# Performance work log

Hardware: AMD Instinct MI355X
Metric: run time of the kernel (lower is better)

## Reference

```python
import jax, jax.numpy as jnp
import numpy as np

T, N, E, IN, HID, H, DK, L, OUT = 2, 16384, 262144, 128, 256, 8, 32, 2, 64
SRC_T, DST_T = (0, 1), (1, 0)
SQRT_DK = float(np.sqrt(DK))


def _gelu(x):
    return jax.nn.gelu(x, approximate=False)


def _seg_softmax(scores, seg, n):
    # edge softmax normalized by destination node (variable in-degree segments)
    m = jax.ops.segment_max(scores, seg, num_segments=n)
    e = jnp.exp(scores - m[seg])
    d = jax.ops.segment_sum(e, seg, num_segments=n)
    return e / d[seg]


def _posvect(x, ww, wb, lw, lb, sw, sb, gw, gb, fw, fb):
    # x: [T,N,6] scalar features; per-(type,modality) weights [T,6,HID]; fw: [T,6,4*HID,HID]
    xe = x[..., None]                                    # [T,N,6,1]
    aff = lambda w, b: xe * w[:, None] + b[:, None]      # [T,N,6,HID]
    acts = (jnp.sin(aff(ww, wb)), aff(lw, lb),
            jax.nn.softplus(aff(sw, sb)), jax.nn.sigmoid(aff(gw, gb)))
    out = fb[:, None]
    for i, a in enumerate(acts):
        out = out + jnp.einsum('tnmh,tmhk->tnmk', a, fw[:, :, i * HID:(i + 1) * HID, :])
    return out                                           # [T,N,6,HID]


def _forward(node_ft, scalars, src_idx, dst_idx, proj_w, proj_b,
             pv_wave_w, pv_wave_b, pv_lin_w, pv_lin_b, pv_sp_w, pv_sp_b,
             pv_sig_w, pv_sig_b, pv_fc_w, pv_fc_b, ima_w1, ima_b1, ima_w2,
             lyr_k_w, lyr_q_w, lyr_v_w, lyr_fc_w, lyr_k_b, lyr_q_b, lyr_v_b,
             lyr_fc_b, lyr_att_w, lyr_val_w, lyr_canon, lyr_res,
             lyr_ln_g, lyr_ln_b, out_w, out_b, sel_node_type):
    # per-type input projection + six positional encodings -> 7 modalities
    h0 = _gelu(jnp.einsum('tnd,tdh->tnh', node_ft, proj_w) + proj_b[:, None])
    pv = _gelu(_posvect(scalars, pv_wave_w, pv_wave_b, pv_lin_w, pv_lin_b,
                        pv_sp_w, pv_sp_b, pv_sig_w, pv_sig_b, pv_fc_w, pv_fc_b))
    z = jnp.concatenate([h0[:, :, None], pv], axis=2)    # [T,N,7,HID]
    w = jnp.tanh(z @ ima_w1 + ima_b1) @ ima_w2           # [T,N,7,1]
    h = (jax.nn.softmax(w, axis=2) * z).sum(2)           # [T,N,HID]
    for l in range(L):
        k = (jnp.einsum('tnd,tdh->tnh', h, lyr_k_w[l]) + lyr_k_b[l][:, None]).reshape(T, N, H, DK)
        q = (jnp.einsum('tnd,tdh->tnh', h, lyr_q_w[l]) + lyr_q_b[l][:, None]).reshape(T, N, H, DK)
        v = (jnp.einsum('tnd,tdh->tnh', h, lyr_v_w[l]) + lyr_v_b[l][:, None]).reshape(T, N, H, DK)
        agg = [None, None]
        for e in range(2):  # canonical etypes: (a->b), (b->a)
            st, dt = SRC_T[e], DST_T[e]
            ke = jnp.einsum('nhi,hij->nhj', k[st], lyr_att_w[l, e])
            ve = jnp.einsum('nhi,hij->nhj', v[st], lyr_val_w[l, e])
            s, d = src_idx[e], dst_idx[e]
            score = (q[dt][d] * ke[s]).sum(-1) * lyr_canon[l, e] / SQRT_DK  # [E,H]
            attn = _seg_softmax(score, d, N)
            agg[dt] = jax.ops.segment_sum(ve[s] * attn[..., None], d, num_segments=N)
        t = jnp.stack(agg).reshape(T, N, HID)  # cross_reducer mean over single etype per dst == identity
        alpha = jax.nn.sigmoid(lyr_res[l])[:, None, None]
        hp = jnp.einsum('tnh,thk->tnk', t, lyr_fc_w[l]) + lyr_fc_b[l][:, None]
        hp = hp * alpha + h * (1.0 - alpha)
        mu = hp.mean(-1, keepdims=True)
        var = ((hp - mu) ** 2).mean(-1, keepdims=True)
        h = (hp - mu) / jnp.sqrt(var + 1e-5) * lyr_ln_g[l][:, None] + lyr_ln_b[l][:, None]
    return h[sel_node_type] @ out_w + out_b


def setup_inputs() -> dict:
    key = jax.random.key(0)
    ks = iter(jax.random.split(key, 64))
    nrm = lambda shape, scale=1.0: jax.random.normal(next(ks), shape, dtype=jnp.float32) * scale
    inp = {}
    inp['node_ft'] = nrm((T, N, IN))
    inp['scalars'] = jax.random.uniform(next(ks), (T, N, 6), dtype=jnp.float32)
    inp['src_idx'] = jax.random.randint(next(ks), (T, E), 0, N, dtype=jnp.int32)
    inp['dst_idx'] = jax.random.randint(next(ks), (T, E), 0, N, dtype=jnp.int32)
    inp['proj_w'] = nrm((T, IN, HID), IN ** -0.5)
    inp['proj_b'] = jnp.zeros((T, HID), jnp.float32)
    for nm in ['pv_wave_w', 'pv_wave_b', 'pv_lin_w', 'pv_lin_b', 'pv_sp_w', 'pv_sp_b', 'pv_sig_w', 'pv_sig_b']:
        inp[nm] = nrm((T, 6, HID))
    inp['pv_fc_w'] = nrm((T, 6, 4 * HID, HID), (4 * HID) ** -0.5)
    inp['pv_fc_b'] = jnp.zeros((T, 6, HID), jnp.float32)
    inp['ima_w1'] = nrm((HID, 128), HID ** -0.5)
    inp['ima_b1'] = jnp.zeros((128,), jnp.float32)
    inp['ima_w2'] = nrm((128, 1), 128 ** -0.5)
    for nm in ['lyr_k_w', 'lyr_q_w', 'lyr_v_w', 'lyr_fc_w']:
        inp[nm] = nrm((L, T, HID, HID), HID ** -0.5)
    for nm in ['lyr_k_b', 'lyr_q_b', 'lyr_v_b', 'lyr_fc_b']:
        inp[nm] = jnp.zeros((L, T, HID), jnp.float32)
    inp['lyr_att_w'] = nrm((L, 2, H, DK, DK), DK ** -0.5)
    inp['lyr_val_w'] = nrm((L, 2, H, DK, DK), DK ** -0.5)
    inp['lyr_canon'] = jnp.ones((L, 2, H), jnp.float32)
    inp['lyr_res'] = jnp.ones((L, T), jnp.float32)
    inp['lyr_ln_g'] = jnp.ones((L, T, HID), jnp.float32)
    inp['lyr_ln_b'] = jnp.zeros((L, T, HID), jnp.float32)
    inp['out_w'] = nrm((HID, OUT), HID ** -0.5)
    inp['out_b'] = jnp.zeros((OUT,), jnp.float32)
    inp['sel_node_type'] = 0
    return inp


def reference(node_ft, scalars, src_idx, dst_idx, proj_w, proj_b,
              pv_wave_w, pv_wave_b, pv_lin_w, pv_lin_b, pv_sp_w, pv_sp_b,
              pv_sig_w, pv_sig_b, pv_fc_w, pv_fc_b, ima_w1, ima_b1, ima_w2,
              lyr_k_w, lyr_q_w, lyr_v_w, lyr_fc_w, lyr_k_b, lyr_q_b, lyr_v_b,
              lyr_fc_b, lyr_att_w, lyr_val_w, lyr_canon, lyr_res,
              lyr_ln_g, lyr_ln_b, out_w, out_b, sel_node_type):
    return _forward(node_ft, scalars, src_idx, dst_idx, proj_w, proj_b,
                    pv_wave_w, pv_wave_b, pv_lin_w, pv_lin_b, pv_sp_w, pv_sp_b,
                    pv_sig_w, pv_sig_b, pv_fc_w, pv_fc_b, ima_w1, ima_b1, ima_w2,
                    lyr_k_w, lyr_q_w, lyr_v_w, lyr_fc_w, lyr_k_b, lyr_q_b, lyr_v_b,
                    lyr_fc_b, lyr_att_w, lyr_val_w, lyr_canon, lyr_res,
                    lyr_ln_g, lyr_ln_b, out_w, out_b, sel_node_type)
```

## Files before the change

kernel.cpp:

```cpp
#include <hip/hip_runtime.h>
#include <hip/hip_bf16.h>

typedef unsigned short u16;
typedef unsigned int   u32;
typedef __attribute__((ext_vector_type(8))) short bf16x8;
typedef __attribute__((ext_vector_type(4))) float f32x4;
typedef __attribute__((ext_vector_type(4))) u16   u16x4;

constexpr int TT  = 2;
constexpr int NN  = 16384;
constexpr int EE  = 262144;

__device__ __forceinline__ u16 f2b(float f){
  u32 x = __float_as_uint(f);
  u32 r = (x + 0x7fffu + ((x >> 16) & 1u)) >> 16;
  return (u16)r;
}
__device__ __forceinline__ float b2f(u16 u){ return __uint_as_float(((u32)u) << 16); }
__device__ __forceinline__ u32 pack2bf(float a, float b){
  __hip_bfloat162 h = __float22bfloat162_rn(make_float2(a, b));
  union { __hip_bfloat162 h2; u32 u; } cv; cv.h2 = h; return cv.u;
}

__device__ __forceinline__ int swz64(int row, int c){
  return (row << 6) + (c ^ ((row & 7) << 3));
}

__device__ __forceinline__ void gl_lds16(const u16* g, u16* l){
  __builtin_amdgcn_global_load_lds(
      (const __attribute__((address_space(1))) u32*)g,
      (__attribute__((address_space(3))) u32*)l, 16, 0, 0);
}

__device__ __forceinline__ float fast_tanh(float u){
  return 1.f - 2.f*__builtin_amdgcn_rcpf(1.f + __expf(2.f*u));
}
__device__ __forceinline__ float gelu_f(float x){
  float u = 0.7978845608028654f * (x + 0.044715f * x*x*x);
  return 0.5f * x * (1.f + fast_tanh(u));
}

__global__ void csr_hist(const int* __restrict__ dst, int* __restrict__ cnt){
  int id = blockIdx.x*256 + threadIdx.x;
  int e = id >> 18;
  atomicAdd(&cnt[e*NN + dst[id]], 1);
}

__global__ void csr_scan(const int* __restrict__ cnt, int* __restrict__ offs){
  const int e = blockIdx.x, tid = threadIdx.x;
  const int CH = NN/256;
  const int* c = cnt + e*NN;
  int* of = offs + e*(NN+1);
  const int base = tid*CH;
  int s = 0;
  for(int i=0;i<CH;i++) s += c[base+i];
  __shared__ int sm[256];
  sm[tid] = s; __syncthreads();
  for(int o=1;o<256;o<<=1){
    int v = (tid>=o) ? sm[tid-o] : 0;
    __syncthreads();
    sm[tid] += v;
    __syncthreads();
  }
  int run = sm[tid] - s;
  for(int i=0;i<CH;i++){ of[base+i] = run; run += c[base+i]; }
  if(tid==255) of[NN] = run;
}

__global__ void csr_scatter(const int* __restrict__ dst, const int* __restrict__ src,
                            const int* __restrict__ offs, int* __restrict__ cur,
                            int* __restrict__ elist){
  int id = blockIdx.x*256 + threadIdx.x;
  int e = id >> 18;
  int d = dst[id];
  int pos = offs[e*(NN+1)+d] + atomicAdd(&cur[e*NN+d], 1);
  elist[e*EE + pos] = src[id];
}

__global__ void tconv(const float* __restrict__ in, u16* __restrict__ out, int K, int Nc){
  __shared__ float tile[32][33];
  const long base = (long)blockIdx.z * K * Nc;
  const int k0 = blockIdx.x*32, n0 = blockIdx.y*32;
  const int tx = threadIdx.x, ty = threadIdx.y;
  for(int i=0;i<32;i+=8)
    tile[ty+i][tx] = in[base + (long)(k0+ty+i)*Nc + n0+tx];
  __syncthreads();
  for(int i=0;i<32;i+=8)
    out[base + (long)(n0+ty+i)*K + k0+tx] = f2b(tile[tx][ty+i]);
}

__global__ void eff_w(const float* __restrict__ kw, const float* __restrict__ vw,
                      const float* __restrict__ kb, const float* __restrict__ vb,
                      const float* __restrict__ att, const float* __restrict__ val,
                      u16* __restrict__ qkvwt, float* __restrict__ qkvb){
  const int h = blockIdx.x, lt = blockIdx.y, kv = blockIdx.z;
  const int l = lt >> 1;
  const float* W = (kv ? vw : kw) + (long)lt*65536;
  const float* A = (kv ? val : att) + (long)lt*8192 + h*1024;
  const float* B = (kv ? vb : kb) + (long)lt*256 + h*32;
  __shared__ float As[32][33];
  for(int idx=threadIdx.x; idx<1024; idx+=256) As[idx>>5][idx&31] = A[idx];
  __syncthreads();
  const int r = threadIdx.x;
  float x[32];
  const float* wr = W + (long)r*256 + h*32;
  #pragma unroll
  for(int i=0;i<32;i++) x[i] = wr[i];
  u16* outb = qkvwt + (kv ? 524288 : 0) + (long)lt*65536;
  #pragma unroll 4
  for(int j=0;j<32;j++){
    float s = 0.f;
    #pragma unroll
    for(int i=0;i<32;i++) s = fmaf(x[i], As[i][j], s);
    outb[(h*32 + j)*256 + r] = f2b(s);
  }
  if (r < 32){
    float s = 0.f;
    #pragma unroll
    for(int i=0;i<32;i++) s = fmaf(B[i], As[i][r], s);
    qkvb[l*1536 + (kv ? 1024 : 0) + (lt&1)*256 + h*32 + r] = s;
  }
}

__global__ void pack_qb(const float* __restrict__ qb, float* __restrict__ qkvb){
  int i = blockIdx.x*256 + threadIdx.x;
  int l = i >> 9, r = i & 511;
  qkvb[l*1536 + 512 + r] = qb[l*512 + r];
}

__global__ void cheb_g(const float* __restrict__ ww, const float* __restrict__ wb,
                       const float* __restrict__ lw, const float* __restrict__ lb,
                       const float* __restrict__ sw, const float* __restrict__ sb,
                       const float* __restrict__ gw, const float* __restrict__ gb,
                       const float* __restrict__ fcw, float* __restrict__ Gpart){
  const int p  = blockIdx.x;
  const int by = blockIdx.y;
  const int s  = p >> 1;
  const int tid = threadIdx.x;
  __shared__ float as_[128][36];
  if (tid < 128){
    const int hl = (p & 1)*128 + tid;
    const float* W = (s==0 ? ww : s==1 ? lw : s==2 ? sw : gw) + by*256;
    const float* B = (s==0 ? wb : s==1 ? lb : s==2 ? sb : gb) + by*256;
    const float w = W[hl], b = B[hl];
    #pragma unroll
    for (int d=0; d<32; d++){
      const float th = ((float)d + 0.5f) * (3.14159265358979323846f/32.f);
      const float x  = 0.5f*cosf(th) + 0.5f;
      const float y  = x*w + b;
      float a;
      if (s==0)      a = sinf(y);
      else if (s==1) a = y;
      else if (s==2) a = fmaxf(y,0.f) + log1pf(expf(-fabsf(y)));
      else           a = 1.f/(1.f + expf(-y));
      as_[tid][d] = a;
    }
  }
  __syncthreads();
  const int k = tid;
  float acc[32];
  #pragma unroll
  for (int d=0; d<32; d++) acc[d] = 0.f;
  const float* fwp = fcw + ((long)by*1024 + p*128)*256 + k;
  for (int hh=0; hh<128; hh++){
    const float f = fwp[(long)hh*256];
    const f32x4* av = (const f32x4*)&as_[hh][0];
    #pragma unroll
    for (int dq=0; dq<8; dq++){
      const f32x4 a4 = av[dq];
      acc[dq*4+0] = fmaf(a4.x, f, acc[dq*4+0]);
      acc[dq*4+1] = fmaf(a4.y, f, acc[dq*4+1]);
      acc[dq*4+2] = fmaf(a4.z, f, acc[dq*4+2]);
      acc[dq*4+3] = fmaf(a4.w, f, acc[dq*4+3]);
    }
  }
  float* gp = Gpart + (long)(by*8 + p)*32*256 + k;
  #pragma unroll
  for (int d=0; d<32; d++) gp[d*256] = acc[d];
}

__global__ void cheb_dct(const float* __restrict__ Gpart, const float* __restrict__ fcb,
                         u16* __restrict__ Cbf, float* __restrict__ c0b){
  const int by = blockIdx.x; const int k = threadIdx.x;
  __shared__ float ct[1024];
  for (int i=k; i<1024; i+=256){
    const int j = i>>5, d = i&31;
    ct[i] = cosf((float)j*((float)d + 0.5f)*(3.14159265358979323846f/32.f));
  }
  __syncthreads();
  float g[32];
  #pragma unroll
  for (int d=0; d<32; d++){
    float s = 0.f;
    #pragma unroll
    for (int p=0; p<8; p++) s += Gpart[(long)(by*8+p)*32*256 + d*256 + k];
    g[d] = s;
  }
  u16* co = Cbf + ((long)by*256 + k)*32;
  #pragma unroll
  for (int j=0; j<32; j++){
    float s = 0.f;
    #pragma unroll
    for (int d=0; d<32; d++) s = fmaf(g[d], ct[j*32+d], s);
    if (j==0){ c0b[by*256+k] = s*(1.f/32.f) + fcb[by*256+k]; co[0] = 0; }
    else co[j] = f2b(s*(1.f/16.f));
  }
}

__global__ void __launch_bounds__(256,2)
posvect2(const float* __restrict__ scalars, const u16* __restrict__ Cbf,
         const float* __restrict__ c0b, u16* __restrict__ zb){
  __shared__ __align__(16) u16 lB[256*40];
  __shared__ float xs[128];
  const int tid = threadIdx.x;
  const int by = blockIdx.y;
  const int t = by / 6, m = by % 6;
  const int m0 = blockIdx.x * 128;
  const int lane = tid & 63, wvi = tid >> 6;
  const int wc0 = wvi * 64;
  const int l16 = lane & 15, qd = lane >> 4;

  if (tid < 128) xs[tid] = scalars[((long)t*NN + m0 + tid)*6 + m];
  const u16* Cb = Cbf + (long)by*8192;
  for (int idx = tid; idx < 1024; idx += 256){
    const int row = idx >> 2, ch = idx & 3;
    *(uint4*)&lB[row*40 + ch*8] = *(const uint4*)&Cb[row*32 + ch*8];
  }
  __syncthreads();

  bf16x8 af[8];
  #pragma unroll
  for (int i=0;i<8;i++){
    const float u = 2.f*xs[i*16 + l16] - 1.f;
    float t0 = 1.f, t1 = u;
    u32 pk[16];
    pk[0] = pack2bf(t0, t1);
    #pragma unroll
    for (int j2=1; j2<16; j2++){
      const float a = 2.f*u*t1 - t0;
      const float b = 2.f*u*a  - t1;
      pk[j2] = pack2bf(a, b);
      t0 = a; t1 = b;
    }
    u32 w[4];
    #pragma unroll
    for (int c=0;c<4;c++){
      const u32 v01 = (qd & 2) ? pk[8+c]  : pk[c];
      const u32 v23 = (qd & 2) ? pk[12+c] : pk[4+c];
      w[c] = (qd & 1) ? v23 : v01;
    }
    union { u32 u4[4]; bf16x8 v; } cv;
    cv.u4[0]=w[0]; cv.u4[1]=w[1]; cv.u4[2]=w[2]; cv.u4[3]=w[3];
    af[i] = cv.v;
  }

  bf16x8 bfr[4];
  #pragma unroll
  for (int jj=0;jj<4;jj++)
    bfr[jj] = *(const bf16x8*)&lB[(wc0 + jj*16 + l16)*40 + qd*8];

  f32x4 acc[8][4];
  #pragma unroll
  for (int i=0;i<8;i++)
    #pragma unroll
    for (int jj=0;jj<4;jj++)
      acc[i][jj] = __builtin_amdgcn_mfma_f32_16x16x32_bf16(
          af[i], bfr[jj], (f32x4){0.f,0.f,0.f,0.f}, 0,0,0);

  u16* zout = zb + ((long)t*NN + m0)*1792 + (m+1)*256;
  #pragma unroll
  for (int i=0;i<8;i++){
    #pragma unroll
    for (int jj=0;jj<4;jj++){
      const int col = wc0 + jj*16 + l16;
      const float bv = c0b[by*256 + col];
      #pragma unroll
      for (int r=0;r<4;r++){
        const int row = i*16 + qd*4 + r;
        zout[(long)row*1792 + col] = f2b(gelu_f(acc[i][jj][r] + bv));
      }
    }
  }
}

template<int BM,int BN,int BK,int WM,int WN,int ASRC,int EPI,int ZQKV>
__global__ void __launch_bounds__(256,2)
gemm_k(const void* __restrict__ Av, const u16* __restrict__ Bt,
       const float* __restrict__ bias, void* Cv,
       int K, int lda, int ldc,
       long strideA, long strideB, long strideBias, long strideC,
       const float* resid, const float* __restrict__ resgate,
       const int* __restrict__ selp, u16* __restrict__ kvout,
       const float* __restrict__ lng, const float* __restrict__ lnb)
{
  static_assert(BK == 64, "swizzle assumes BK=64");
  constexpr int WTM = BM/WM, WTN = BN/WN;
  constexpr int RM = WTM/16, RN = WTN/16;
  __shared__ __align__(16) u16 lA[BM*64];
  __shared__ __align__(16) u16 lB[BN*64];

  const int tid = threadIdx.x;
  const int by  = blockIdx.y;
  const int m0  = blockIdx.x * BM;
  const int lane = tid & 63, wvi = tid >> 6;
  const int wr = wvi / WN, wc = wvi % WN;
  const int wr0 = wr * WTM, wc0 = wc * WTN;
  const int l16 = lane & 15, qd = lane >> 4;
  const int csrc = (((lane & 7) ^ (lane >> 3)) << 3);

  int zq = 0; int boff = 0;
  if constexpr (ZQKV){
    zq = blockIdx.z;
    boff = zq*512;
  }

  long aoff = (long)by * strideA;
  if (selp) aoff += (long)selp[0] * strideA;
  const float* A32 = (const float*)Av;
  const u16*   A16 = (const u16*)Av;
  const u16*   Bp  = Bt + (long)by * strideB + (long)zq * 262144;

  f32x4 acc[RM][RN];
  #pragma unroll
  for(int i=0;i<RM;i++)
    #pragma unroll
    for(int j=0;j<RN;j++) acc[i][j] = (f32x4){0.f,0.f,0.f,0.f};

  for(int k0=0;k0<K;k0+=BK){
    if constexpr (ASRC == 0){
      for(int idx=tid; idx < BM*16; idx += 256){
        int r = idx >> 4, c = (idx & 15)*4;
        const float4 v = *(const float4*)(A32 + aoff + (long)(m0+r)*lda + k0 + c);
        uint2 o2; o2.x = pack2bf(v.x, v.y); o2.y = pack2bf(v.z, v.w);
        *(uint2*)&lA[swz64(r, c)] = o2;
      }
    } else {
      #pragma unroll
      for(int ch = wvi; ch < BM/8; ch += 4){
        const int r = ch*8 + (lane>>3);
        gl_lds16(A16 + aoff + (long)(m0+r)*lda + k0 + csrc, &lA[ch*512]);
      }
    }
    #pragma unroll
    for(int ch = wvi; ch < BN/8; ch += 4){
      const int n = ch*8 + (lane>>3);
      gl_lds16(Bp + (long)n*K + k0 + csrc, &lB[ch*512]);
    }
    __syncthreads();
    #pragma unroll
    for(int ks=0; ks<BK; ks+=32){
      bf16x8 af[RM], bfr[RN];
      #pragma unroll
      for(int i=0;i<RM;i++) af[i]  = *(const bf16x8*)&lA[swz64(wr0 + i*16 + l16, ks + qd*8)];
      #pragma unroll
      for(int j=0;j<RN;j++) bfr[j] = *(const bf16x8*)&lB[swz64(wc0 + j*16 + l16, ks + qd*8)];
      #pragma unroll
      for(int i=0;i<RM;i++)
        #pragma unroll
        for(int j=0;j<RN;j++)
          acc[i][j] = __builtin_amdgcn_mfma_f32_16x16x32_bf16(af[i], bfr[j], acc[i][j], 0,0,0);
    }
    __syncthreads();
  }

  if constexpr (EPI == 4){
    float* rsum = (float*)lA;
    #pragma unroll
    for(int i=0;i<RM;i++){
      #pragma unroll
      for(int r=0;r<4;r++){
        float part = 0.f;
        #pragma unroll
        for(int jj=0;jj<RN;jj++){
          const int col = wc0 + jj*16 + l16;
          const float v = fast_tanh(acc[i][jj][r] + bias[boff + col]);
          part += v * resid[col];
        }
        part += __shfl_xor(part,1); part += __shfl_xor(part,2);
        part += __shfl_xor(part,4); part += __shfl_xor(part,8);
        if (l16 == 0) rsum[wc*BM + wr0 + i*16 + qd*4 + r] = part;
      }
    }
    __syncthreads();
    if (tid < BM){
      float s = 0.f;
      #pragma unroll
      for(int w=0;w<WN;w++) s += rsum[w*BM + tid];
      ((float*)Cv)[m0 + tid] = s;
    }
    return;
  } else if constexpr (EPI == 5){
    float* red1 = (float*)lA;
    float* red2 = red1 + WN*BM;
    float* muv  = red2 + WN*BM;
    const float alpha = 1.f/(1.f + __expf(-resgate[by]));
    #pragma unroll
    for(int i=0;i<RM;i++){
      #pragma unroll
      for(int r=0;r<4;r++){
        const int rloc = wr0 + i*16 + qd*4 + r;
        const int row = m0 + rloc;
        float s1 = 0.f, s2 = 0.f;
        #pragma unroll
        for(int j=0;j<RN;j++){
          const int col = wc0 + j*16 + l16;
          float v = acc[i][j][r] + bias[(long)by*strideBias + col];
          const float hv = resid[(long)by*strideC + (long)row*ldc + col];
          v = v*alpha + hv*(1.f - alpha);
          acc[i][j][r] = v;
          s1 += v; s2 += v*v;
        }
        s1 += __shfl_xor(s1,1); s1 += __shfl_xor(s1,2); s1 += __shfl_xor(s1,4); s1 += __shfl_xor(s1,8);
        s2 += __shfl_xor(s2,1); s2 += __shfl_xor(s2,2); s2 += __shfl_xor(s2,4); s2 += __shfl_xor(s2,8);
        if (l16 == 0){ red1[wc*BM + rloc] = s1; red2[wc*BM + rloc] = s2; }
      }
    }
    __syncthreads();
    if (tid < BM){
      float s1 = 0.f, s2 = 0.f;
      #pragma unroll
      for(int w=0;w<WN;w++){ s1 += red1[w*BM + tid]; s2 += red2[w*BM + tid]; }
      const float mu = s1*(1.f/256.f);
      const float var = s2*(1.f/256.f) - mu*mu;
      muv[tid*2]   = mu;
      muv[tid*2+1] = rsqrtf(fmaxf(var, 0.f) + 1e-5f);
    }
    __syncthreads();
    #pragma unroll
    for(int i=0;i<RM;i++){
      #pragma unroll
      for(int r=0;r<4;r++){
        const int rloc = wr0 + i*16 + qd*4 + r;
        const int row = m0 + rloc;
        const float mu = muv[rloc*2], rs = muv[rloc*2+1];
        #pragma unroll
        for(int j=0;j<RN;j++){
          const int col = wc0 + j*16 + l16;
          const float o = (acc[i][j][r]-mu)*rs*lng[by*256+col] + lnb[by*256+col];
          ((float*)Cv)[(long)by*strideC + (long)row*ldc + col] = o;
        }
      }
    }
    return;
  } else {
    #pragma unroll
    for(int i=0;i<RM;i++){
      #pragma unroll
      for(int j=0;j<RN;j++){
        const int col = wc0 + j*16 + l16;
        const float bv = bias[(long)by*strideBias + boff + col];
        #pragma unroll
        for(int r=0;r<4;r++){
          const int row = m0 + wr0 + i*16 + qd*4 + r;
          float v = acc[i][j][r] + bv;
          if constexpr (ZQKV){
            if (zq == 1)
              ((u16*)Cv)[(long)by*strideC + (long)row*ldc + col] = f2b(v);
            else
              kvout[((long)by*NN + row)*512 + ((col>>2)<<3) + (zq==2 ? 4 : 0) + (col&3)] = f2b(v);
          } else {
            const long cidx = (long)by*strideC + (long)row*ldc + col;
            if constexpr (EPI == 0) ((float*)Cv)[cidx] = v;
            else ((u16*)Cv)[cidx] = f2b(gelu_f(v));
          }
        }
      }
    }
  }
}

__global__ void ima_combine(const u16* __restrict__ zb, const float* __restrict__ wbuf,
                            float* __restrict__ H){
  const int row = blockIdx.x*4 + (threadIdx.x>>6);
  const int lane = threadIdx.x & 63;
  const float* w7 = wbuf + (long)row*7;
  float w[7]; float mx = -1e30f;
  #pragma unroll
  for(int m=0;m<7;m++){ w[m] = w7[m]; mx = fmaxf(mx, w[m]); }
  float sum = 0.f;
  #pragma unroll
  for(int m=0;m<7;m++){ w[m] = __expf(w[m]-mx); sum += w[m]; }
  const float inv = __builtin_amdgcn_rcpf(sum);
  float4 acc = {0,0,0,0};
  #pragma unroll
  for(int m=0;m<7;m++){
    const u16x4 z4 = *(const u16x4*)&zb[((long)row*7 + m)*256 + lane*4];
    const float p = w[m]*inv;
    acc.x += p*b2f(z4.x); acc.y += p*b2f(z4.y); acc.z += p*b2f(z4.z); acc.w += p*b2f(z4.w);
  }
  *(float4*)&H[(long)row*256 + lane*4] = acc;
}

__global__ void attn_agg(const u16* __restrict__ Q16, const u16* __restrict__ KV,
                         u16* __restrict__ AGG,
                         const int* __restrict__ offs, const int* __restrict__ elist,
                         const float* __restrict__ canon){
  const int e = blockIdx.y, dt = 1 - e;
  const int d = blockIdx.x*4 + (threadIdx.x>>6);
  const int lane = threadIdx.x & 63;
  const float scale = canon[e*8 + (lane>>3)] * 0.17677669529663687f;

  const uint2 qv = *(const uint2*)&Q16[((long)dt*NN + d)*256 + lane*4];
  const float q0 = b2f((u16)(qv.x&0xffff)), q1 = b2f((u16)(qv.x>>16));
  const float q2 = b2f((u16)(qv.y&0xffff)), q3 = b2f((u16)(qv.y>>16));

  const int p0 = offs[e*(NN+1) + d], p1 = offs[e*(NN+1) + d + 1];
  const int* el = elist + (long)e*EE;
  const u16* KVb = KV + (long)e*NN*512;

  float a0=0.f, a1=0.f, a2=0.f, a3=0.f;
  float den = 0.f;

  auto process = [&](const uint4 kv){
    float dp = q0*b2f((u16)(kv.x&0xffff)) + q1*b2f((u16)(kv.x>>16))
             + q2*b2f((u16)(kv.y&0xffff)) + q3*b2f((u16)(kv.y>>16));
    dp += __shfl_xor(dp,1); dp += __shfl_xor(dp,2); dp += __shfl_xor(dp,4);
    const float w = __expf(dp*scale);
    den += w;
    a0 = fmaf(w, b2f((u16)(kv.z&0xffff)), a0);
    a1 = fmaf(w, b2f((u16)(kv.z>>16)),    a1);
    a2 = fmaf(w, b2f((u16)(kv.w&0xffff)), a2);
    a3 = fmaf(w, b2f((u16)(kv.w>>16)),    a3);
  };

  int p = p0;
  for(; p+8 <= p1; p += 8){
    uint4 kv[8];
    #pragma unroll
    for(int u=0;u<8;u++) kv[u] = *(const uint4*)&KVb[(long)el[p+u]*512 + lane*8];
    #pragma unroll
    for(int u=0;u<8;u++) process(kv[u]);
  }
  for(; p+2 <= p1; p += 2){
    const uint4 a = *(const uint4*)&KVb[(long)el[p]*512 + lane*8];
    const uint4 b = *(const uint4*)&KVb[(long)el[p+1]*512 + lane*8];
    process(a); process(b);
  }
  if (p < p1){
    const uint4 a = *(const uint4*)&KVb[(long)el[p]*512 + lane*8];
    process(a);
  }

  uint2 o = {0,0};
  if (p1 > p0){
    const float r = 1.f/den;
    o.x = pack2bf(a0*r, a1*r);
    o.y = pack2bf(a2*r, a3*r);
  }
  *(uint2*)&AGG[((long)dt*NN + d)*256 + lane*4] = o;
}

extern "C" void kernel_launch(void* const* d_in, const int* in_sizes, int n_in,
                              void* d_out, int out_size, void* d_ws, size_t ws_size,
                              hipStream_t stream) {
  const float* node_ft = (const float*)d_in[0];
  const float* scalars = (const float*)d_in[1];
  const int*   src_idx = (const int*)d_in[2];
  const int*   dst_idx = (const int*)d_in[3];
  const float* proj_w  = (const float*)d_in[4];
  const float* proj_b  = (const float*)d_in[5];
  const float* pv_ww   = (const float*)d_in[6];
  const float* pv_wb   = (const float*)d_in[7];
  const float* pv_lw   = (const float*)d_in[8];
  const float* pv_lb   = (const float*)d_in[9];
  const float* pv_sw   = (const float*)d_in[10];
  const float* pv_sb   = (const float*)d_in[11];
  const float* pv_gw   = (const float*)d_in[12];
  const float* pv_gb   = (const float*)d_in[13];
  const float* pv_fcw  = (const float*)d_in[14];
  const float* pv_fcb  = (const float*)d_in[15];
  const float* ima_w1  = (const float*)d_in[16];
  const float* ima_b1  = (const float*)d_in[17];
  const float* ima_w2  = (const float*)d_in[18];
  const float* lyr_k_w = (const float*)d_in[19];
  const float* lyr_q_w = (const float*)d_in[20];
  const float* lyr_v_w = (const float*)d_in[21];
  const float* lyr_fc_w= (const float*)d_in[22];
  const float* lyr_k_b = (const float*)d_in[23];
  const float* lyr_q_b = (const float*)d_in[24];
  const float* lyr_v_b = (const float*)d_in[25];
  const float* lyr_fc_b= (const float*)d_in[26];
  const float* lyr_att_w=(const float*)d_in[27];
  const float* lyr_val_w=(const float*)d_in[28];
  const float* lyr_canon=(const float*)d_in[29];
  const float* lyr_res = (const float*)d_in[30];
  const float* lyr_ln_g= (const float*)d_in[31];
  const float* lyr_ln_b= (const float*)d_in[32];
  const float* out_w   = (const float*)d_in[33];
  const float* out_b   = (const float*)d_in[34];
  const int*   sel     = (const int*)d_in[35];
  float* outp = (float*)d_out;

  char* ws = (char*)d_ws;
  size_t o = 0;
  auto alloc = [&](size_t bytes)->char*{ char* p = ws + o; o = (o + bytes + 255) & ~(size_t)255; return p; };

  int*   cnt    = (int*)  alloc(2*NN*4);
  int*   cur    = (int*)  alloc(2*NN*4);
  int*   offs   = (int*)  alloc(2*(NN+1)*4);
  int*   elist  = (int*)  alloc(2*EE*4);
  u16*   projwt = (u16*)  alloc((size_t)TT*128*256*2);
  u16*   imaw1t = (u16*)  alloc((size_t)256*128*2);
  u16*   qkvwt  = (u16*)  alloc((size_t)3*262144*2);
  u16*   fcwt   = (u16*)  alloc((size_t)4*256*256*2);
  u16*   outwt  = (u16*)  alloc((size_t)64*256*2);
  float* hbuf   = (float*)alloc((size_t)TT*NN*256*4);
  float* wbuf   = (float*)alloc((size_t)TT*NN*7*4);
  float* Gpart  = (float*)alloc((size_t)12*8*32*256*4);
  u16*   Cbf    = (u16*)  alloc((size_t)12*256*32*2);
  float* c0b    = (float*)alloc((size_t)12*256*4);
  float* qkvb   = (float*)alloc((size_t)TT*3*2*256*4);
  char*  arena  = alloc((size_t)176160768);
  if (o > ws_size) return;

  u16*   zbuf  = (u16*)arena;
  u16*   Qb16  = (u16*)arena;
  u16*   KVb   = (u16*)(arena + 16777216);
  u16*   AGG16 = (u16*)(arena + 50331648);

  hipMemsetAsync(cnt, 0, 2*NN*4, stream);
  hipMemsetAsync(cur, 0, 2*NN*4, stream);
  csr_hist   <<<2*EE/256, 256, 0, stream>>>(dst_idx, cnt);
  csr_scan   <<<2, 256, 0, stream>>>(cnt, offs);
  csr_scatter<<<2*EE/256, 256, 0, stream>>>(dst_idx, src_idx, offs, cur, elist);

  tconv<<<dim3( 4,8, 2), dim3(32,8), 0, stream>>>(proj_w,   projwt, 128, 256);
  tconv<<<dim3( 8,4, 1), dim3(32,8), 0, stream>>>(ima_w1,   imaw1t, 256, 128);
  tconv<<<dim3( 8,8, 4), dim3(32,8), 0, stream>>>(lyr_q_w,  qkvwt + 262144, 256, 256);
  tconv<<<dim3( 8,8, 4), dim3(32,8), 0, stream>>>(lyr_fc_w, fcwt,   256, 256);
  tconv<<<dim3( 8,2, 1), dim3(32,8), 0, stream>>>(out_w,    outwt,  256, 64);
  eff_w<<<dim3(8,4,2), 256, 0, stream>>>(lyr_k_w, lyr_v_w, lyr_k_b, lyr_v_b,
                                         lyr_att_w, lyr_val_w, qkvwt, qkvb);
  pack_qb<<<4, 256, 0, stream>>>(lyr_q_b, qkvb);

  cheb_g  <<<dim3(8,12), 256, 0, stream>>>(pv_ww, pv_wb, pv_lw, pv_lb,
                                           pv_sw, pv_sb, pv_gw, pv_gb, pv_fcw, Gpart);
  cheb_dct<<<12, 256, 0, stream>>>(Gpart, pv_fcb, Cbf, c0b);

  gemm_k<64,256,64,1,4,0,1,0><<<dim3(256,TT), 256, 0, stream>>>(
      node_ft, projwt, proj_b, zbuf, 128, 128, 1792,
      (long)NN*128, 32768L, 256L, (long)NN*1792, nullptr, nullptr, nullptr, nullptr,
      nullptr, nullptr);

  posvect2<<<dim3(128,12), 256, 0, stream>>>(scalars, Cbf, c0b, zbuf);

  gemm_k<64,128,64,2,2,1,4,0><<<dim3(3584,1), 256, 0, stream>>>(
      zbuf, imaw1t, ima_b1, wbuf, 256, 256, 0,
      0L, 0L, 0L, 0L, ima_w2, nullptr, nullptr, nullptr, nullptr, nullptr);
  ima_combine<<<TT*NN/4, 256, 0, stream>>>(zbuf, wbuf, hbuf);

  for (int l = 0; l < 2; ++l){
    gemm_k<64,256,64,1,4,0,0,1><<<dim3(256,TT,3), 256, 0, stream>>>(
        hbuf, qkvwt + (size_t)l*131072, qkvb + (size_t)l*1536, Qb16, 256, 256, 256,
        (long)NN*256, 65536L, 256L, (long)NN*256, nullptr, nullptr, nullptr, KVb,
        nullptr, nullptr);

    attn_agg<<<dim3(NN/4, 2), 256, 0, stream>>>(Qb16, KVb, AGG16, offs, elist,
                                                lyr_canon + l*2*8);

    gemm_k<64,256,64,1,4,1,5,0><<<dim3(256,TT), 256, 0, stream>>>(
        AGG16, fcwt + (size_t)l*2*65536, lyr_fc_b + l*2*256, hbuf, 256, 256, 256,
        (long)NN*256, 65536L, 256L, (long)NN*256, hbuf, lyr_res + l*2, nullptr, nullptr,
        lyr_ln_g + l*2*256, lyr_ln_b + l*2*256);
  }

  gemm_k<256,64,64,4,1,0,0,0><<<dim3(64,1), 256, 0, stream>>>(
      hbuf, outwt, out_b, outp, 256, 256, 64,
      (long)NN*256, 0L, 0L, 0L, nullptr, nullptr, sel, nullptr, nullptr, nullptr);

  (void)in_sizes; (void)n_in; (void)out_size;
}
```

Measured before the change: 684.4 us.

## Split cheb_g over Chebyshev degrees and stage posvect2 output through LDS

cheb_g gets a third grid dimension that splits the 32 Chebyshev degrees into four groups of eight, giving four times as many blocks and fewer accumulators per thread. The posvect2 epilogue now writes the GELU'd bf16 results into shared memory (reusing the B tile buffer) in 32-row chunks and then stores them to global with 16-byte coalesced writes, instead of scattered 2-byte stores. The cost is extra __syncthreads, LDS round trips, and recomputing the activations four times in cheb_g.

```diff
diff --git a/kernel.cpp b/kernel.cpp
--- a/kernel.cpp
+++ b/kernel.cpp
@@ -135,16 +135,18 @@
                        const float* __restrict__ fcw, float* __restrict__ Gpart){
   const int p  = blockIdx.x;
   const int by = blockIdx.y;
+  const int zg = blockIdx.z;
   const int s  = p >> 1;
   const int tid = threadIdx.x;
-  __shared__ float as_[128][36];
+  __shared__ float as_[128][9];
   if (tid < 128){
     const int hl = (p & 1)*128 + tid;
     const float* W = (s==0 ? ww : s==1 ? lw : s==2 ? sw : gw) + by*256;
     const float* B = (s==0 ? wb : s==1 ? lb : s==2 ? sb : gb) + by*256;
     const float w = W[hl], b = B[hl];
     #pragma unroll
-    for (int d=0; d<32; d++){
+    for (int dd=0; dd<8; dd++){
+      const int d = zg*8 + dd;
       const float th = ((float)d + 0.5f) * (3.14159265358979323846f/32.f);
       const float x  = 0.5f*cosf(th) + 0.5f;
       const float y  = x*w + b;
@@ -153,30 +155,23 @@
       else if (s==1) a = y;
       else if (s==2) a = fmaxf(y,0.f) + log1pf(expf(-fabsf(y)));
       else           a = 1.f/(1.f + expf(-y));
-      as_[tid][d] = a;
+      as_[tid][dd] = a;
     }
   }
   __syncthreads();
   const int k = tid;
-  float acc[32];
-  #pragma unroll
-  for (int d=0; d<32; d++) acc[d] = 0.f;
+  float acc[8];
+  #pragma unroll
+  for (int dd=0; dd<8; dd++) acc[dd] = 0.f;
   const float* fwp = fcw + ((long)by*1024 + p*128)*256 + k;
   for (int hh=0; hh<128; hh++){
     const float f = fwp[(long)hh*256];
-    const f32x4* av = (const f32x4*)&as_[hh][0];
-    #pragma unroll
-    for (int dq=0; dq<8; dq++){
-      const f32x4 a4 = av[dq];
-      acc[dq*4+0] = fmaf(a4.x, f, acc[dq*4+0]);
-      acc[dq*4+1] = fmaf(a4.y, f, acc[dq*4+1]);
-      acc[dq*4+2] = fmaf(a4.z, f, acc[dq*4+2]);
-      acc[dq*4+3] = fmaf(a4.w, f, acc[dq*4+3]);
-    }
-  }
-  float* gp = Gpart + (long)(by*8 + p)*32*256 + k;
-  #pragma unroll
-  for (int d=0; d<32; d++) gp[d*256] = acc[d];
+    #pragma unroll
+    for (int dd=0; dd<8; dd++) acc[dd] = fmaf(as_[hh][dd], f, acc[dd]);
+  }
+  float* gp = Gpart + (long)(by*8 + p)*32*256 + (long)(zg*8)*256 + k;
+  #pragma unroll
+  for (int dd=0; dd<8; dd++) gp[dd*256] = acc[dd];
 }
 
 __global__ void cheb_dct(const float* __restrict__ Gpart, const float* __restrict__ fcb,
@@ -267,18 +262,35 @@
       acc[i][jj] = __builtin_amdgcn_mfma_f32_16x16x32_bf16(
           af[i], bfr[jj], (f32x4){0.f,0.f,0.f,0.f}, 0,0,0);
 
+  float bvj[4];
+  #pragma unroll
+  for (int jj=0;jj<4;jj++) bvj[jj] = c0b[by*256 + wc0 + jj*16 + l16];
+
+  u16* st = (u16*)lB;
   u16* zout = zb + ((long)t*NN + m0)*1792 + (m+1)*256;
   #pragma unroll
-  for (int i=0;i<8;i++){
-    #pragma unroll
-    for (int jj=0;jj<4;jj++){
-      const int col = wc0 + jj*16 + l16;
-      const float bv = c0b[by*256 + col];
-      #pragma unroll
-      for (int r=0;r<4;r++){
-        const int row = i*16 + qd*4 + r;
-        zout[(long)row*1792 + col] = f2b(gelu_f(acc[i][jj][r] + bv));
+  for (int c=0;c<4;c++){
+    __syncthreads();
+    #pragma unroll
+    for (int ii=0;ii<2;ii++){
+      const int i = c*2 + ii;
+      #pragma unroll
+      for (int jj=0;jj<4;jj++){
+        const int col = wc0 + jj*16 + l16;
+        #pragma unroll
+        for (int r=0;r<4;r++){
+          const int rowl = ii*16 + qd*4 + r;
+          st[rowl*264 + col] = f2b(gelu_f(acc[i][jj][r] + bvj[jj]));
+        }
       }
+    }
+    __syncthreads();
+    #pragma unroll
+    for (int it=0; it<4; it++){
+      const int f = it*256 + tid;
+      const int rowl = f >> 5, seg = f & 31;
+      const uint4 v = *(const uint4*)&st[rowl*264 + seg*8];
+      *(uint4*)&zout[(long)(c*32 + rowl)*1792 + seg*8] = v;
     }
   }
 }
@@ -633,8 +645,8 @@
                                          lyr_att_w, lyr_val_w, qkvwt, qkvb);
   pack_qb<<<4, 256, 0, stream>>>(lyr_q_b, qkvb);
 
-  cheb_g  <<<dim3(8,12), 256, 0, stream>>>(pv_ww, pv_wb, pv_lw, pv_lb,
-                                           pv_sw, pv_sb, pv_gw, pv_gb, pv_fcw, Gpart);
+  cheb_g  <<<dim3(8,12,4), 256, 0, stream>>>(pv_ww, pv_wb, pv_lw, pv_lb,
+                                             pv_sw, pv_sb, pv_gw, pv_gb, pv_fcw, Gpart);
   cheb_dct<<<12, 256, 0, stream>>>(Gpart, pv_fcb, Cbf, c0b);
 
   gemm_k<64,256,64,1,4,0,1,0><<<dim3(256,TT), 256, 0, stream>>>(
```

Measured after the change: 661.9 us. 3.3% less time.
